# Kernel tuning notes

Measured on AMD Instinct MI355X. Metric: run time of the kernel, lower is better.

The kernel has to match this reference:

```python
import jax, jax.numpy as jnp
import numpy as np

N1, N2, D = 2048, 2048, 64  # d_q_in=d_q_out=d_k_in=d_k_out=d_v=64


def setup_inputs() -> dict:
    key = jax.random.key(0)
    ks = jax.random.split(key, 9)
    s = 0.05
    return {
        "q": jax.random.normal(ks[0], (N1, D), dtype=jnp.float32),
        "k": jax.random.normal(ks[1], (N2, D), dtype=jnp.float32),
        "v": jax.random.normal(ks[2], (N2, D), dtype=jnp.float32),
        # q_w: Linear(d_q_in -> d_q_out)
        "Wq": jax.random.normal(ks[3], (D, D), dtype=jnp.float32) * s,
        "bq": jax.random.normal(ks[4], (D,), dtype=jnp.float32) * s,
        # k_w: Linear(d_k_in -> d_k_out)
        "Wk": jax.random.normal(ks[5], (D, D), dtype=jnp.float32) * s,
        "bk": jax.random.normal(ks[6], (D,), dtype=jnp.float32) * s,
        # w: Linear(d_q_out -> 1)
        "w": jax.random.normal(ks[7], (D,), dtype=jnp.float32) * s,
        "b": jax.random.normal(ks[8], (1,), dtype=jnp.float32) * s,
    }


def reference(q, k, v, Wq, bq, Wk, bk, w, b):
    # x' = w3 * sigma(w1*q + w2*k); Bahdanau-style additive attention.
    qp = q @ Wq + bq                      # [N1, D]
    kp = k @ Wk + bk                      # [N2, D]
    h = jax.nn.sigmoid(qp[:, None, :] + kp[None, :, :])   # [N1, N2, D]
    att_score = jnp.einsum("nmd,d->nm", h, w) + b[0]       # [N1, N2]
    att_weight = jax.nn.softmax(att_score, axis=-1)
    output = att_weight @ v               # [N1, D]
    return (output, att_score)
```

## Files before the change

### kernel.cpp

```cpp
#include <hip/hip_runtime.h>
#include <math.h>

#define N1 2048
#define N2 2048
#define DD 64
#define NJ 10
#define KDIM (DD*NJ)
#define NKS (KDIM/32)

static constexpr float LOG2E = 1.4426950408889634f;
static constexpr float ACLIP = 2.6f;

typedef _Float16 f16x8 __attribute__((ext_vector_type(8)));
typedef float    f32x4 __attribute__((ext_vector_type(4)));

__device__ const float XNODE_dev[NJ] = {
     2.5679897f,  2.3166170f,  1.8384776f,  1.1803753f,  0.4067296f,
    -0.4067296f, -1.1803753f, -1.8384776f, -2.3166170f, -2.5679897f };
__device__ const float WBAR_dev[NJ] = {
     1.4751660e-3f, -4.2811330e-3f,  6.6679880e-3f, -8.4021590e-3f,
     9.3138610e-3f, -9.3138610e-3f,  8.4021590e-3f, -6.6679880e-3f,
     4.2811330e-3f, -1.4751660e-3f };

__global__ __launch_bounds__(256) void k_proj2(
    const float* __restrict__ q, const float* __restrict__ k,
    const float* __restrict__ Wq, const float* __restrict__ bq,
    const float* __restrict__ Wk, const float* __restrict__ bk,
    float* __restrict__ qp, float* __restrict__ kp)
{
    int bx = blockIdx.x;
    bool is_q = bx < 512;
    int row0 = (is_q ? bx : bx - 512) * 4;
    const float* X = is_q ? q : k;
    const float* W = is_q ? Wq : Wk;
    const float* bias = is_q ? bq : bk;

    __shared__ float xrow[4][64];
    int t = threadIdx.x;
    int wv = t >> 6, lane = t & 63;
    xrow[wv][lane] = X[(row0 + wv) * DD + lane];
    __syncthreads();

    float acc = 0.f;
    #pragma unroll
    for (int j = 0; j < 64; ++j)
        acc = fmaf(xrow[wv][j], W[j * DD + lane], acc);

    float val = acc + bias[lane];
    int row = row0 + wv;
    if (is_q) qp[row * DD + lane] = val;
    else      kp[row * DD + lane] = val;
}

__global__ __launch_bounds__(256) void k_prep_a(
    const float* __restrict__ qp, const float* __restrict__ w,
    f16x8* __restrict__ Ap)
{
    int slot = blockIdx.x * 256 + threadIdx.x;
    int mt = blockIdx.y;
    int ks = slot >> 6;
    int lane = slot & 63;
    int row = mt * 16 + (lane & 15);
    int kbase = ks * 32 + (lane >> 4) * 8;

    f16x8 o;
    #pragma unroll
    for (int jj = 0; jj < 8; ++jj) {
        int kk = kbase + jj;
        int d = (kk * 6554) >> 16;
        int j = kk - d * 10;
        float a = qp[row * DD + d];
        a = fminf(fmaxf(a, -ACLIP), ACLIP);
        float p = WBAR_dev[j];
        #pragma unroll
        for (int i = 0; i < NJ; ++i) {
            float df = a - XNODE_dev[i];
            p *= (i == j) ? 1.0f : df;
        }
        o[jj] = (_Float16)(p * w[d]);
    }
    Ap[(mt * NKS + ks) * 64 + lane] = o;
}

__global__ __launch_bounds__(256) void k_prep_b(
    const float* __restrict__ kp, f16x8* __restrict__ Bp)
{
    int slot = blockIdx.x * 256 + threadIdx.x;
    int nt = blockIdx.y;
    int ks = slot >> 6;
    int lane = slot & 63;
    int col = nt * 16 + (lane & 15);
    int kbase = ks * 32 + (lane >> 4) * 8;

    f16x8 o;
    #pragma unroll
    for (int jj = 0; jj < 8; ++jj) {
        int kk = kbase + jj;
        int d = (kk * 6554) >> 16;
        int j = kk - d * 10;
        float s = XNODE_dev[j] + kp[col * DD + d];
        float sg = __builtin_amdgcn_rcpf(1.0f + __builtin_amdgcn_exp2f(-s * LOG2E));
        o[jj] = (_Float16)sg;
    }
    Bp[(nt * NKS + ks) * 64 + lane] = o;
}

__global__ __launch_bounds__(256) void k_gemm(
    const f16x8* __restrict__ Ap, const f16x8* __restrict__ Bp,
    const float* __restrict__ bscal, float* __restrict__ score)
{
    int bx = blockIdx.x;
    int mb = bx >> 5;
    int nb = bx & 31;
    int t = threadIdx.x, wv = t >> 6, lane = t & 63;
    int mt0 = mb * 8 + wv * 2;
    int nt0 = nb * 4;

    const f16x8* pA0 = Ap + (mt0 * NKS) * 64 + lane;
    const f16x8* pA1 = pA0 + NKS * 64;
    const f16x8* pB  = Bp + (nt0 * NKS) * 64 + lane;

    f32x4 acc[2][4] = {};
    f16x8 af[2], bf[4], afn[2], bfn[4];
    af[0] = pA0[0];  af[1] = pA1[0];
    bf[0] = pB[0];   bf[1] = pB[NKS * 64];
    bf[2] = pB[2 * NKS * 64];  bf[3] = pB[3 * NKS * 64];

    for (int ks = 0; ks < NKS; ++ks) {
        int nx = (ks + 1 < NKS ? ks + 1 : ks) * 64;
        afn[0] = pA0[nx];  afn[1] = pA1[nx];
        bfn[0] = pB[nx];               bfn[1] = pB[NKS * 64 + nx];
        bfn[2] = pB[2 * NKS * 64 + nx]; bfn[3] = pB[3 * NKS * 64 + nx];
        #pragma unroll
        for (int i = 0; i < 2; ++i)
            #pragma unroll
            for (int c = 0; c < 4; ++c)
                acc[i][c] = __builtin_amdgcn_mfma_f32_16x16x32_f16(
                    af[i], bf[c], acc[i][c], 0, 0, 0);
        af[0] = afn[0]; af[1] = afn[1];
        bf[0] = bfn[0]; bf[1] = bfn[1]; bf[2] = bfn[2]; bf[3] = bfn[3];
    }

    float bias = bscal[0];
    #pragma unroll
    for (int i = 0; i < 2; ++i) {
        int rowb = (mt0 + i) * 16 + (lane >> 4) * 4;
        #pragma unroll
        for (int c = 0; c < 4; ++c) {
            int col = (nt0 + c) * 16 + (lane & 15);
            #pragma unroll
            for (int r = 0; r < 4; ++r)
                score[(rowb + r) * N2 + col] = acc[i][c][r] + bias;
        }
    }
}

__global__ __launch_bounds__(256) void k_out(
    const float* __restrict__ score, const float* __restrict__ v,
    float* __restrict__ out)
{
    int n0 = blockIdx.x * 4;
    __shared__ float p_lds[4][2048];
    __shared__ float red[4][4];
    __shared__ float part[4][4][64];
    __shared__ float inv_s[4];
    int t = threadIdx.x, wv = t >> 6, lane = t & 63;

    float psum[4];
    #pragma unroll
    for (int r = 0; r < 4; ++r) {
        psum[r] = 0.f;
        #pragma unroll
        for (int kk = 0; kk < 2; ++kk) {
            int m4 = t + 256 * kk;
            float4 s4 = ((const float4*)(score + (n0 + r) * N2))[m4];
            float4 p4;
            p4.x = __builtin_amdgcn_exp2f(s4.x * LOG2E);
            p4.y = __builtin_amdgcn_exp2f(s4.y * LOG2E);
            p4.z = __builtin_amdgcn_exp2f(s4.z * LOG2E);
            p4.w = __builtin_amdgcn_exp2f(s4.w * LOG2E);
            *(float4*)&p_lds[r][m4 * 4] = p4;
            psum[r] += p4.x + p4.y + p4.z + p4.w;
        }
    }
    #pragma unroll
    for (int r = 0; r < 4; ++r) {
        float x = psum[r];
        #pragma unroll
        for (int off = 32; off > 0; off >>= 1)
            x += __shfl_down(x, off, 64);
        if (lane == 0) red[r][wv] = x;
    }
    __syncthreads();
    if (t < 4)
        inv_s[t] = 1.0f / (red[t][0] + red[t][1] + red[t][2] + red[t][3]);
    __syncthreads();

    int m_off = lane >> 4, d4 = lane & 15;
    const float4* v4 = (const float4*)v;
    float4 a[4] = {{0,0,0,0},{0,0,0,0},{0,0,0,0},{0,0,0,0}};
    int mstart = wv * 512;
    #pragma unroll 4
    for (int i = 0; i < 128; ++i) {
        int m = mstart + i * 4 + m_off;
        float4 vv = v4[m * 16 + d4];
        #pragma unroll
        for (int r = 0; r < 4; ++r) {
            float p = p_lds[r][m];
            a[r].x = fmaf(p, vv.x, a[r].x);
            a[r].y = fmaf(p, vv.y, a[r].y);
            a[r].z = fmaf(p, vv.z, a[r].z);
            a[r].w = fmaf(p, vv.w, a[r].w);
        }
    }
    #pragma unroll
    for (int r = 0; r < 4; ++r) {
        #pragma unroll
        for (int off = 16; off <= 32; off <<= 1) {
            a[r].x += __shfl_xor(a[r].x, off, 64);
            a[r].y += __shfl_xor(a[r].y, off, 64);
            a[r].z += __shfl_xor(a[r].z, off, 64);
            a[r].w += __shfl_xor(a[r].w, off, 64);
        }
    }
    if (lane < 16) {
        #pragma unroll
        for (int r = 0; r < 4; ++r)
            *(float4*)&part[wv][r][d4 * 4] = a[r];
    }
    __syncthreads();
    {
        int r = t >> 6, d = t & 63;
        float s = part[0][r][d] + part[1][r][d] + part[2][r][d] + part[3][r][d];
        out[(n0 + r) * DD + d] = s * inv_s[r];
    }
}

typedef float v2f __attribute__((ext_vector_type(2)));

__global__ __launch_bounds__(256) void k_proj_old(
    const float* __restrict__ q, const float* __restrict__ k,
    const float* __restrict__ Wq, const float* __restrict__ bq,
    const float* __restrict__ Wk, const float* __restrict__ bk,
    float* __restrict__ qp, float* __restrict__ kpT)
{
    int bx = blockIdx.x;
    bool is_q = bx < 512;
    int row0 = (is_q ? bx : bx - 512) * 4;
    const float* X = is_q ? q : k;
    const float* W = is_q ? Wq : Wk;
    const float* bias = is_q ? bq : bk;

    __shared__ float xrow[4][64];
    int t = threadIdx.x;
    int wv = t >> 6, lane = t & 63;
    xrow[wv][lane] = X[(row0 + wv) * DD + lane];
    __syncthreads();

    float acc = 0.f;
    #pragma unroll
    for (int j = 0; j < 64; ++j)
        acc = fmaf(xrow[wv][j], W[j * DD + lane], acc);

    float val = -(acc + bias[lane]) * LOG2E;
    int row = row0 + wv;
    if (is_q) qp[row * DD + lane] = val;
    else      kpT[lane * N2 + row] = val;
}

__global__ __launch_bounds__(256, 8) void k_score_old(
    const float* __restrict__ qp, const float* __restrict__ kpT,
    const float* __restrict__ w, const float* __restrict__ b,
    float* __restrict__ score)
{
    int bx = blockIdx.x;
    int n0 = (bx >> 3) * 8;
    int m_base = (bx & 7) * 256;

    __shared__ float qp_s[8][64];
    __shared__ float w_s[64];
    int t = threadIdx.x;
    if (t < 128)
        ((float4*)qp_s)[t] = ((const float4*)(qp + n0 * DD))[t];
    if (t < 64) w_s[t] = w[t];
    float b0 = b[0];
    __syncthreads();

    int rgrp = t >> 6, lane = t & 63;
    int r0 = rgrp * 2;
    int m0 = m_base + lane * 4;

    v2f acc2[2][2];
    #pragma unroll
    for (int i2 = 0; i2 < 2; ++i2)
        #pragma unroll
        for (int jp = 0; jp < 2; ++jp)
            acc2[i2][jp] = (v2f){b0, b0};

    const float* kbase = kpT + m0;

    for (int d0 = 0; d0 < 64; d0 += 4) {
        float4 kv[4];
        #pragma unroll
        for (int dd = 0; dd < 4; ++dd)
            kv[dd] = *(const float4*)(kbase + (d0 + dd) * N2);

        float4 wvv = *(const float4*)&w_s[d0];
        #pragma unroll
        for (int i2 = 0; i2 < 2; ++i2) {
            float4 qv = *(const float4*)&qp_s[r0 + i2][d0];
            #pragma unroll
            for (int dd = 0; dd < 4; ++dd) {
                float qvd = (&qv.x)[dd];
                float wd  = (&wvv.x)[dd];
                v2f q2 = (v2f){qvd, qvd};
                v2f w2 = (v2f){wd, wd};
                v2f klo = (v2f){(&kv[dd].x)[0], (&kv[dd].x)[1]};
                v2f khi = (v2f){(&kv[dd].x)[2], (&kv[dd].x)[3]};
                v2f xlo = q2 + klo;
                v2f xhi = q2 + khi;
                v2f elo, ehi;
                elo.x = __builtin_amdgcn_exp2f(xlo.x);
                elo.y = __builtin_amdgcn_exp2f(xlo.y);
                ehi.x = __builtin_amdgcn_exp2f(xhi.x);
                ehi.y = __builtin_amdgcn_exp2f(xhi.y);
                v2f dlo = elo + (v2f){1.f, 1.f};
                v2f dhi = ehi + (v2f){1.f, 1.f};
                v2f slo, shi;
                slo.x = __builtin_amdgcn_rcpf(dlo.x);
                slo.y = __builtin_amdgcn_rcpf(dlo.y);
                shi.x = __builtin_amdgcn_rcpf(dhi.x);
                shi.y = __builtin_amdgcn_rcpf(dhi.y);
                acc2[i2][0] = __builtin_elementwise_fma(w2, slo, acc2[i2][0]);
                acc2[i2][1] = __builtin_elementwise_fma(w2, shi, acc2[i2][1]);
            }
        }
    }

    #pragma unroll
    for (int i2 = 0; i2 < 2; ++i2) {
        float4 o = { acc2[i2][0].x, acc2[i2][0].y,
                     acc2[i2][1].x, acc2[i2][1].y };
        *(float4*)&score[(n0 + r0 + i2) * N2 + m0] = o;
    }
}

extern "C" void kernel_launch(void* const* d_in, const int* in_sizes, int n_in,
                              void* d_out, int out_size, void* d_ws, size_t ws_size,
                              hipStream_t stream) {
    const float* q  = (const float*)d_in[0];
    const float* k  = (const float*)d_in[1];
    const float* v  = (const float*)d_in[2];
    const float* Wq = (const float*)d_in[3];
    const float* bq = (const float*)d_in[4];
    const float* Wk = (const float*)d_in[5];
    const float* bk = (const float*)d_in[6];
    const float* w  = (const float*)d_in[7];
    const float* b  = (const float*)d_in[8];

    float* out   = (float*)d_out;
    float* score = out + N1 * DD;

    const size_t PACKED = (size_t)2048 * KDIM * 2;
    const size_t NEED = 1048576 + 2 * PACKED;

    if (ws_size >= NEED) {
        float* qp = (float*)d_ws;
        float* kp = qp + N1 * DD;
        f16x8* Ap = (f16x8*)((char*)d_ws + 1048576);
        f16x8* Bp = (f16x8*)((char*)d_ws + 1048576 + PACKED);

        k_proj2 <<<1024, 256, 0, stream>>>(q, k, Wq, bq, Wk, bk, qp, kp);
        k_prep_a<<<dim3(5, 128), 256, 0, stream>>>(qp, w, Ap);
        k_prep_b<<<dim3(5, 128), 256, 0, stream>>>(kp, Bp);
        k_gemm  <<<512, 256, 0, stream>>>(Ap, Bp, b, score);
        k_out   <<<512, 256, 0, stream>>>(score, v, out);
    } else {
        float* qp  = (float*)d_ws;
        float* kpT = qp + N1 * DD;
        k_proj_old <<<1024, 256, 0, stream>>>(q, k, Wq, bq, Wk, bk, qp, kpT);
        k_score_old<<<2048, 256, 0, stream>>>(qp, kpT, w, b, score);
        k_out      <<<512, 256, 0, stream>>>(score, v, out);
    }
}
```

Baseline: 117.6 us.

## Fuse projection and operand packing into one kernel, deepen GEMM prefetch

Merges the three kernels for the Q/K projections and the A/B operand packing into a single kernel. Each block projects 16 rows into LDS and then writes the packed fp16 operands directly, which removes two launches and the qp/kp workspace round trip. The MFMA GEMM now keeps a three-stage register prefetch ring with a fully unrolled k-loop in place of single-step prefetch, which raises register pressure. k_out interleaves probabilities in LDS in pairs so one vector load serves two rows, and the unused fallback score kernel is rewritten in scalar form.

```diff
diff --git a/kernel.cpp b/kernel.cpp
--- a/kernel.cpp
+++ b/kernel.cpp
@@ -13,6 +13,7 @@
 
 typedef _Float16 f16x8 __attribute__((ext_vector_type(8)));
 typedef float    f32x4 __attribute__((ext_vector_type(4)));
+typedef float    v2f   __attribute__((ext_vector_type(2)));
 
 __device__ const float XNODE_dev[NJ] = {
      2.5679897f,  2.3166170f,  1.8384776f,  1.1803753f,  0.4067296f,
@@ -22,87 +23,97 @@
      9.3138610e-3f, -9.3138610e-3f,  8.4021590e-3f, -6.6679880e-3f,
      4.2811330e-3f, -1.4751660e-3f };
 
-__global__ __launch_bounds__(256) void k_proj2(
+__global__ __launch_bounds__(256) void k_prep(
     const float* __restrict__ q, const float* __restrict__ k,
     const float* __restrict__ Wq, const float* __restrict__ bq,
     const float* __restrict__ Wk, const float* __restrict__ bk,
-    float* __restrict__ qp, float* __restrict__ kp)
-{
-    int bx = blockIdx.x;
-    bool is_q = bx < 512;
-    int row0 = (is_q ? bx : bx - 512) * 4;
-    const float* X = is_q ? q : k;
-    const float* W = is_q ? Wq : Wk;
+    const float* __restrict__ w,
+    f16x8* __restrict__ Ap, f16x8* __restrict__ Bp)
+{
+    int t = threadIdx.x;
+    bool is_q = blockIdx.x < 128;
+    int rb = is_q ? blockIdx.x : (blockIdx.x - 128);
+    int row0 = rb * 16;
+    const float* X    = is_q ? q : k;
+    const float* W    = is_q ? Wq : Wk;
     const float* bias = is_q ? bq : bk;
 
-    __shared__ float xrow[4][64];
-    int t = threadIdx.x;
-    int wv = t >> 6, lane = t & 63;
-    xrow[wv][lane] = X[(row0 + wv) * DD + lane];
-    __syncthreads();
-
-    float acc = 0.f;
-    #pragma unroll
-    for (int j = 0; j < 64; ++j)
-        acc = fmaf(xrow[wv][j], W[j * DD + lane], acc);
-
-    float val = acc + bias[lane];
-    int row = row0 + wv;
-    if (is_q) qp[row * DD + lane] = val;
-    else      kp[row * DD + lane] = val;
-}
-
-__global__ __launch_bounds__(256) void k_prep_a(
-    const float* __restrict__ qp, const float* __restrict__ w,
-    f16x8* __restrict__ Ap)
-{
-    int slot = blockIdx.x * 256 + threadIdx.x;
-    int mt = blockIdx.y;
-    int ks = slot >> 6;
-    int lane = slot & 63;
-    int row = mt * 16 + (lane & 15);
-    int kbase = ks * 32 + (lane >> 4) * 8;
-
-    f16x8 o;
-    #pragma unroll
-    for (int jj = 0; jj < 8; ++jj) {
-        int kk = kbase + jj;
-        int d = (kk * 6554) >> 16;
-        int j = kk - d * 10;
-        float a = qp[row * DD + d];
-        a = fminf(fmaxf(a, -ACLIP), ACLIP);
-        float p = WBAR_dev[j];
-        #pragma unroll
-        for (int i = 0; i < NJ; ++i) {
-            float df = a - XNODE_dev[i];
-            p *= (i == j) ? 1.0f : df;
-        }
-        o[jj] = (_Float16)(p * w[d]);
-    }
-    Ap[(mt * NKS + ks) * 64 + lane] = o;
-}
-
-__global__ __launch_bounds__(256) void k_prep_b(
-    const float* __restrict__ kp, f16x8* __restrict__ Bp)
-{
-    int slot = blockIdx.x * 256 + threadIdx.x;
-    int nt = blockIdx.y;
-    int ks = slot >> 6;
-    int lane = slot & 63;
-    int col = nt * 16 + (lane & 15);
-    int kbase = ks * 32 + (lane >> 4) * 8;
-
-    f16x8 o;
-    #pragma unroll
-    for (int jj = 0; jj < 8; ++jj) {
-        int kk = kbase + jj;
-        int d = (kk * 6554) >> 16;
-        int j = kk - d * 10;
-        float s = XNODE_dev[j] + kp[col * DD + d];
-        float sg = __builtin_amdgcn_rcpf(1.0f + __builtin_amdgcn_exp2f(-s * LOG2E));
-        o[jj] = (_Float16)sg;
-    }
-    Bp[(nt * NKS + ks) * 64 + lane] = o;
+    __shared__ float4 xs4[16][17];
+    __shared__ float  pp[16][66];
+    __shared__ float  wls[64];
+    __shared__ float  xn_s[NJ], wb_s[NJ];
+
+    {
+        int r = t >> 4, c4 = t & 15;
+        xs4[r][c4] = *(const float4*)&X[(row0 + r) * DD + c4 * 4];
+    }
+    if (t < 64) wls[t] = w[t];
+    if (t >= 64 && t < 64 + NJ) xn_s[t - 64] = XNODE_dev[t - 64];
+    if (t >= 96 && t < 96 + NJ) wb_s[t - 96] = WBAR_dev[t - 96];
+    __syncthreads();
+
+    {
+        int col = t & 63, rbase = t >> 6;
+        float acc[4];
+        float bv = bias[col];
+        acc[0] = acc[1] = acc[2] = acc[3] = bv;
+        #pragma unroll
+        for (int j4 = 0; j4 < 16; ++j4) {
+            float wj[4];
+            #pragma unroll
+            for (int jj = 0; jj < 4; ++jj)
+                wj[jj] = W[(j4 * 4 + jj) * DD + col];
+            #pragma unroll
+            for (int i = 0; i < 4; ++i) {
+                float4 xv = xs4[rbase + 4 * i][j4];
+                acc[i] = fmaf(xv.x, wj[0], acc[i]);
+                acc[i] = fmaf(xv.y, wj[1], acc[i]);
+                acc[i] = fmaf(xv.z, wj[2], acc[i]);
+                acc[i] = fmaf(xv.w, wj[3], acc[i]);
+            }
+        }
+        #pragma unroll
+        for (int i = 0; i < 4; ++i)
+            pp[rbase + 4 * i][col] = acc[i];
+    }
+    __syncthreads();
+
+    #pragma unroll
+    for (int s = 0; s < 5; ++s) {
+        int slot = t + 256 * s;
+        int ks = slot >> 6, lane = slot & 63;
+        int row = lane & 15;
+        int kbase = ks * 32 + (lane >> 4) * 8;
+        f16x8 o;
+        if (is_q) {
+            #pragma unroll
+            for (int jj = 0; jj < 8; ++jj) {
+                int kk = kbase + jj;
+                int d = (kk * 6554) >> 16;
+                int j = kk - d * 10;
+                float a = pp[row][d];
+                a = fminf(fmaxf(a, -ACLIP), ACLIP);
+                float p = wb_s[j];
+                #pragma unroll
+                for (int i = 0; i < NJ; ++i)
+                    p *= (i == j) ? 1.0f : (a - xn_s[i]);
+                o[jj] = (_Float16)(p * wls[d]);
+            }
+            Ap[(rb * NKS + ks) * 64 + lane] = o;
+        } else {
+            #pragma unroll
+            for (int jj = 0; jj < 8; ++jj) {
+                int kk = kbase + jj;
+                int d = (kk * 6554) >> 16;
+                int j = kk - d * 10;
+                float sv = xn_s[j] + pp[row][d];
+                float sg = __builtin_amdgcn_rcpf(
+                    1.0f + __builtin_amdgcn_exp2f(-sv * LOG2E));
+                o[jj] = (_Float16)sg;
+            }
+            Bp[(rb * NKS + ks) * 64 + lane] = o;
+        }
+    }
 }
 
 __global__ __launch_bounds__(256) void k_gemm(
@@ -116,29 +127,37 @@
     int mt0 = mb * 8 + wv * 2;
     int nt0 = nb * 4;
 
-    const f16x8* pA0 = Ap + (mt0 * NKS) * 64 + lane;
-    const f16x8* pA1 = pA0 + NKS * 64;
-    const f16x8* pB  = Bp + (nt0 * NKS) * 64 + lane;
+    const int ST = NKS * 64;
+    const f16x8* pA0 = Ap + mt0 * ST + lane;
+    const f16x8* pA1 = pA0 + ST;
+    const f16x8* pB  = Bp + nt0 * ST + lane;
 
     f32x4 acc[2][4] = {};
-    f16x8 af[2], bf[4], afn[2], bfn[4];
-    af[0] = pA0[0];  af[1] = pA1[0];
-    bf[0] = pB[0];   bf[1] = pB[NKS * 64];
-    bf[2] = pB[2 * NKS * 64];  bf[3] = pB[3 * NKS * 64];
-
+    f16x8 buf[3][6];
+
+    auto load_step = [&](int ks, f16x8* dst) {
+        int off = ks * 64;
+        dst[0] = pA0[off];
+        dst[1] = pA1[off];
+        dst[2] = pB[off];
+        dst[3] = pB[ST + off];
+        dst[4] = pB[2 * ST + off];
+        dst[5] = pB[3 * ST + off];
+    };
+    load_step(0, buf[0]);
+    load_step(1, buf[1]);
+    load_step(2, buf[2]);
+
+    #pragma unroll
     for (int ks = 0; ks < NKS; ++ks) {
-        int nx = (ks + 1 < NKS ? ks + 1 : ks) * 64;
-        afn[0] = pA0[nx];  afn[1] = pA1[nx];
-        bfn[0] = pB[nx];               bfn[1] = pB[NKS * 64 + nx];
-        bfn[2] = pB[2 * NKS * 64 + nx]; bfn[3] = pB[3 * NKS * 64 + nx];
+        f16x8* cur = buf[ks % 3];
         #pragma unroll
         for (int i = 0; i < 2; ++i)
             #pragma unroll
             for (int c = 0; c < 4; ++c)
                 acc[i][c] = __builtin_amdgcn_mfma_f32_16x16x32_f16(
-                    af[i], bf[c], acc[i][c], 0, 0, 0);
-        af[0] = afn[0]; af[1] = afn[1];
-        bf[0] = bfn[0]; bf[1] = bfn[1]; bf[2] = bfn[2]; bf[3] = bfn[3];
+                    cur[i], cur[2 + c], acc[i][c], 0, 0, 0);
+        if (ks + 3 < NKS) load_step(ks + 3, cur);
     }
 
     float bias = bscal[0];
@@ -160,7 +179,7 @@
     float* __restrict__ out)
 {
     int n0 = blockIdx.x * 4;
-    __shared__ float p_lds[4][2048];
+    __shared__ float p_lds[2][2048][2];
     __shared__ float red[4][4];
     __shared__ float part[4][4][64];
     __shared__ float inv_s[4];
@@ -170,17 +189,13 @@
     #pragma unroll
     for (int r = 0; r < 4; ++r) {
         psum[r] = 0.f;
-        #pragma unroll
-        for (int kk = 0; kk < 2; ++kk) {
-            int m4 = t + 256 * kk;
-            float4 s4 = ((const float4*)(score + (n0 + r) * N2))[m4];
-            float4 p4;
-            p4.x = __builtin_amdgcn_exp2f(s4.x * LOG2E);
-            p4.y = __builtin_amdgcn_exp2f(s4.y * LOG2E);
-            p4.z = __builtin_amdgcn_exp2f(s4.z * LOG2E);
-            p4.w = __builtin_amdgcn_exp2f(s4.w * LOG2E);
-            *(float4*)&p_lds[r][m4 * 4] = p4;
-            psum[r] += p4.x + p4.y + p4.z + p4.w;
+        const float* srow = score + (n0 + r) * N2;
+        #pragma unroll
+        for (int kk = 0; kk < 8; ++kk) {
+            int m = t + 256 * kk;
+            float p = __builtin_amdgcn_exp2f(srow[m] * LOG2E);
+            p_lds[r >> 1][m][r & 1] = p;
+            psum[r] += p;
         }
     }
     #pragma unroll
@@ -203,15 +218,17 @@
     #pragma unroll 4
     for (int i = 0; i < 128; ++i) {
         int m = mstart + i * 4 + m_off;
+        v2f p01 = *(const v2f*)&p_lds[0][m][0];
+        v2f p23 = *(const v2f*)&p_lds[1][m][0];
         float4 vv = v4[m * 16 + d4];
-        #pragma unroll
-        for (int r = 0; r < 4; ++r) {
-            float p = p_lds[r][m];
-            a[r].x = fmaf(p, vv.x, a[r].x);
-            a[r].y = fmaf(p, vv.y, a[r].y);
-            a[r].z = fmaf(p, vv.z, a[r].z);
-            a[r].w = fmaf(p, vv.w, a[r].w);
-        }
+        a[0].x = fmaf(p01.x, vv.x, a[0].x);  a[0].y = fmaf(p01.x, vv.y, a[0].y);
+        a[0].z = fmaf(p01.x, vv.z, a[0].z);  a[0].w = fmaf(p01.x, vv.w, a[0].w);
+        a[1].x = fmaf(p01.y, vv.x, a[1].x);  a[1].y = fmaf(p01.y, vv.y, a[1].y);
+        a[1].z = fmaf(p01.y, vv.z, a[1].z);  a[1].w = fmaf(p01.y, vv.w, a[1].w);
+        a[2].x = fmaf(p23.x, vv.x, a[2].x);  a[2].y = fmaf(p23.x, vv.y, a[2].y);
+        a[2].z = fmaf(p23.x, vv.z, a[2].z);  a[2].w = fmaf(p23.x, vv.w, a[2].w);
+        a[3].x = fmaf(p23.y, vv.x, a[3].x);  a[3].y = fmaf(p23.y, vv.y, a[3].y);
+        a[3].z = fmaf(p23.y, vv.z, a[3].z);  a[3].w = fmaf(p23.y, vv.w, a[3].w);
     }
     #pragma unroll
     for (int r = 0; r < 4; ++r) {
@@ -235,8 +252,6 @@
         out[(n0 + r) * DD + d] = s * inv_s[r];
     }
 }
-
-typedef float v2f __attribute__((ext_vector_type(2)));
 
 __global__ __launch_bounds__(256) void k_proj_old(
     const float* __restrict__ q, const float* __restrict__ k,
@@ -290,12 +305,12 @@
     int r0 = rgrp * 2;
     int m0 = m_base + lane * 4;
 
-    v2f acc2[2][2];
+    float acc[2][4];
     #pragma unroll
     for (int i2 = 0; i2 < 2; ++i2)
         #pragma unroll
-        for (int jp = 0; jp < 2; ++jp)
-            acc2[i2][jp] = (v2f){b0, b0};
+        for (int j = 0; j < 4; ++j)
+            acc[i2][j] = b0;
 
     const float* kbase = kpT + m0;
 
@@ -313,34 +328,20 @@
             for (int dd = 0; dd < 4; ++dd) {
                 float qvd = (&qv.x)[dd];
                 float wd  = (&wvv.x)[dd];
-                v2f q2 = (v2f){qvd, qvd};
-                v2f w2 = (v2f){wd, wd};
-                v2f klo = (v2f){(&kv[dd].x)[0], (&kv[dd].x)[1]};
-                v2f khi = (v2f){(&kv[dd].x)[2], (&kv[dd].x)[3]};
-                v2f xlo = q2 + klo;
-                v2f xhi = q2 + khi;
-                v2f elo, ehi;
-                elo.x = __builtin_amdgcn_exp2f(xlo.x);
-                elo.y = __builtin_amdgcn_exp2f(xlo.y);
-                ehi.x = __builtin_amdgcn_exp2f(xhi.x);
-                ehi.y = __builtin_amdgcn_exp2f(xhi.y);
-                v2f dlo = elo + (v2f){1.f, 1.f};
-                v2f dhi = ehi + (v2f){1.f, 1.f};
-                v2f slo, shi;
-                slo.x = __builtin_amdgcn_rcpf(dlo.x);
-                slo.y = __builtin_amdgcn_rcpf(dlo.y);
-                shi.x = __builtin_amdgcn_rcpf(dhi.x);
-                shi.y = __builtin_amdgcn_rcpf(dhi.y);
-                acc2[i2][0] = __builtin_elementwise_fma(w2, slo, acc2[i2][0]);
-                acc2[i2][1] = __builtin_elementwise_fma(w2, shi, acc2[i2][1]);
+                #pragma unroll
+                for (int j = 0; j < 4; ++j) {
+                    float x = qvd + (&kv[dd].x)[j];
+                    float e = __builtin_amdgcn_exp2f(x);
+                    float sg = __builtin_amdgcn_rcpf(1.0f + e);
+                    acc[i2][j] = fmaf(wd, sg, acc[i2][j]);
+                }
             }
         }
     }
 
     #pragma unroll
     for (int i2 = 0; i2 < 2; ++i2) {
-        float4 o = { acc2[i2][0].x, acc2[i2][0].y,
-                     acc2[i2][1].x, acc2[i2][1].y };
+        float4 o = { acc[i2][0], acc[i2][1], acc[i2][2], acc[i2][3] };
         *(float4*)&score[(n0 + r0 + i2) * N2 + m0] = o;
     }
 }
@@ -362,19 +363,14 @@
     float* score = out + N1 * DD;
 
     const size_t PACKED = (size_t)2048 * KDIM * 2;
-    const size_t NEED = 1048576 + 2 * PACKED;
-
-    if (ws_size >= NEED) {
-        float* qp = (float*)d_ws;
-        float* kp = qp + N1 * DD;
-        f16x8* Ap = (f16x8*)((char*)d_ws + 1048576);
-        f16x8* Bp = (f16x8*)((char*)d_ws + 1048576 + PACKED);
-
-        k_proj2 <<<1024, 256, 0, stream>>>(q, k, Wq, bq, Wk, bk, qp, kp);
-        k_prep_a<<<dim3(5, 128), 256, 0, stream>>>(qp, w, Ap);
-        k_prep_b<<<dim3(5, 128), 256, 0, stream>>>(kp, Bp);
-        k_gemm  <<<512, 256, 0, stream>>>(Ap, Bp, b, score);
-        k_out   <<<512, 256, 0, stream>>>(score, v, out);
+
+    if (ws_size >= 2 * PACKED) {
+        f16x8* Ap = (f16x8*)d_ws;
+        f16x8* Bp = (f16x8*)((char*)d_ws + PACKED);
+
+        k_prep<<<256, 256, 0, stream>>>(q, k, Wq, bq, Wk, bk, w, Ap, Bp);
+        k_gemm<<<512, 256, 0, stream>>>(Ap, Bp, b, score);
+        k_out <<<512, 256, 0, stream>>>(score, v, out);
     } else {
         float* qp  = (float*)d_ws;
         float* kpT = qp + N1 * DD;
```

After: 113.5 us. -3.5%, faster.
